# Optimization experiments

Hardware: AMD Instinct MI355X
Metric: run time of the kernel (lower is better)

Reference implementation:

```python
import jax, jax.numpy as jnp
import numpy as np
import math

D_MODEL = 512
N_HEADS = 8
BMIN, BMAX = 0.3, 1.0
W_E, W_M, W_I = 0.4, 0.4, 0.2


def norm_minmax(t):
    t_min = t.min(axis=-1, keepdims=True)
    t_max = t.max(axis=-1, keepdims=True)
    return (t - t_min) / jnp.maximum(t_max - t_min, 1e-8)


def setup_inputs() -> dict:
    key = jax.random.key(0)
    ks = jax.random.split(key, 12)
    B, S, D, C = 2, 2048, D_MODEL, 1000
    x = jax.random.normal(ks[0], (B, S, D), dtype=jnp.float32)
    out_probs = jax.nn.softmax(jax.random.normal(ks[1], (B, C), dtype=jnp.float32), axis=-1)
    idf_seq = jax.random.uniform(ks[2], (B, S), dtype=jnp.float32)
    def lin(kw, kb):
        W = jax.random.normal(kw, (D, D), dtype=jnp.float32) * 0.02
        b = jax.random.normal(kb, (D,), dtype=jnp.float32) * 0.02
        return W, b
    Wq, bq = lin(ks[3], ks[4])
    Wk, bk = lin(ks[5], ks[6])
    Wv, bv = lin(ks[7], ks[8])
    Wo, bo = lin(ks[9], ks[10])
    return dict(x=x, out_probs=out_probs, idf_seq=idf_seq,
                Wq=Wq, bq=bq, Wk=Wk, bk=bk, Wv=Wv, bv=bv, Wo=Wo, bo=bo)


def reference(x, out_probs, idf_seq, Wq, bq, Wk, bk, Wv, bv, Wo, bo):
    B, S, D = x.shape
    H = N_HEADS
    dk = D // H

    def heads(W, b):
        # (B,S,D) -> (B,H,S,dk)
        return (x @ W.T + b).reshape(B, S, H, dk).swapaxes(1, 2)

    q = heads(Wq, bq)
    k = heads(Wk, bk)
    v = heads(Wv, bv)

    logits = jnp.einsum('bhqd,bhkd->bhqk', q, k) / math.sqrt(dk)
    attn_probs = jax.nn.softmax(logits, axis=-1)  # (B,H,S,S)

    # --- compute_load ---
    p = jnp.maximum(attn_probs, 1e-12)
    H_i = (-(p * jnp.log(p)).sum(axis=-1)).mean(axis=1)  # (B,S)
    H_i = norm_minmax(H_i)

    top2 = jax.lax.top_k(out_probs, 2)[0]  # (B,2)
    margin = jnp.maximum(top2[:, 0] - top2[:, 1], 0.0)[:, None]  # (B,1)
    margin = jnp.broadcast_to(margin, (B, S))
    margin = norm_minmax(margin)
    load_from_margin = 1.0 - margin

    L = W_E * H_i + W_M * load_from_margin + W_I * idf_seq
    L = norm_minmax(L)

    # --- map load to budget and cap ---
    Bgt = BMIN + (BMAX - BMIN) * L  # (B,S)
    row_sum = jnp.maximum(attn_probs.sum(axis=-1, keepdims=True), 1e-12)  # (B,H,S,1)
    scale = jnp.minimum(Bgt[:, None, :, None] / row_sum, 1.0)
    attn_probs = attn_probs * scale

    y = jnp.einsum('bhqk,bhkd->bhqd', attn_probs, v)  # (B,H,S,dk)
    y = y.swapaxes(1, 2).reshape(B, S, D)
    y = y @ Wo.T + bo
    return y, attn_probs
```

## Files before the change

### kernel.cpp

```cpp
#include <hip/hip_runtime.h>
#include <hip/hip_bf16.h>


typedef __attribute__((ext_vector_type(8))) short bf16x8;
typedef __attribute__((ext_vector_type(4))) float f32x4;

static __device__ __forceinline__ unsigned short f2b(float f) {
  union { float f; unsigned int u; } v; v.f = f;
  unsigned int u = v.u;
  u += 0x7FFF + ((u >> 16) & 1);
  return (unsigned short)(u >> 16);
}

__global__ __launch_bounds__(256) void cvt_all(
    const float* __restrict__ x,
    const float* __restrict__ Wq, const float* __restrict__ Wk,
    const float* __restrict__ Wv, const float* __restrict__ Wo,
    unsigned short* __restrict__ xb, unsigned short* __restrict__ wqkv,
    unsigned short* __restrict__ wob)
{
  int i = blockIdx.x * 256 + threadIdx.x;
  const float* s; unsigned short* d; int off;
  if (i < 524288) { s = x; d = xb; off = i; }
  else {
    int j = i - 524288; int w = j >> 16; off = j & 65535;
    switch (w) {
      case 0: s = Wq; d = wqkv; break;
      case 1: s = Wk; d = wqkv + 262144; break;
      case 2: s = Wv; d = wqkv + 524288; break;
      default: s = Wo; d = wob; break;
    }
  }
  float4 v = reinterpret_cast<const float4*>(s)[off];
  ushort4 o;
  o.x = f2b(v.x); o.y = f2b(v.y); o.z = f2b(v.z); o.w = f2b(v.w);
  reinterpret_cast<ushort4*>(d)[off] = o;
}

__global__ __launch_bounds__(256) void qkv_gemm(
    const unsigned short* __restrict__ xb, const unsigned short* __restrict__ w,
    const float* __restrict__ bq, const float* __restrict__ bk, const float* __restrict__ bv,
    unsigned short* __restrict__ Qb, unsigned short* __restrict__ Kb,
    unsigned short* __restrict__ Vtb)
{
  __shared__ unsigned short smem[5120];
  unsigned short* shA = smem;
  unsigned short* shB = smem + 2560;
  const int tid = threadIdx.x;
  const int bm = blockIdx.x, bn = blockIdx.y;
  const int lane = tid & 63, wid = tid >> 6;
  const int wr = wid >> 1, wc = wid & 1;
  const int lg = lane >> 4, lc = lane & 15;

  f32x4 acc[2][2];
#pragma unroll
  for (int i = 0; i < 2; ++i)
#pragma unroll
    for (int j = 0; j < 2; ++j) acc[i][j] = f32x4{0.f, 0.f, 0.f, 0.f};

  const int row_st = tid >> 2;
  const int k8 = (tid & 3) * 8;
  for (int kt = 0; kt < 16; ++kt) {
    *reinterpret_cast<uint4*>(&shA[row_st * 40 + k8]) =
        *reinterpret_cast<const uint4*>(&xb[(size_t)(bm * 64 + row_st) * 512 + kt * 32 + k8]);
    *reinterpret_cast<uint4*>(&shB[row_st * 40 + k8]) =
        *reinterpret_cast<const uint4*>(&w[(size_t)(bn * 64 + row_st) * 512 + kt * 32 + k8]);
    __syncthreads();
    bf16x8 af[2], bfr[2];
#pragma unroll
    for (int f = 0; f < 2; ++f) {
      af[f]  = *reinterpret_cast<const bf16x8*>(&shA[(wr * 32 + f * 16 + lc) * 40 + lg * 8]);
      bfr[f] = *reinterpret_cast<const bf16x8*>(&shB[(wc * 32 + f * 16 + lc) * 40 + lg * 8]);
    }
#pragma unroll
    for (int fm = 0; fm < 2; ++fm)
#pragma unroll
      for (int fn = 0; fn < 2; ++fn)
        acc[fm][fn] = __builtin_amdgcn_mfma_f32_16x16x32_bf16(af[fm], bfr[fn], acc[fm][fn], 0, 0, 0);
    __syncthreads();
  }

  if (bn < 16) {
#pragma unroll
    for (int fm = 0; fm < 2; ++fm)
#pragma unroll
      for (int fn = 0; fn < 2; ++fn)
#pragma unroll
        for (int r = 0; r < 4; ++r) {
          int mi = bm * 64 + wr * 32 + fm * 16 + lg * 4 + r;
          int ni = bn * 64 + wc * 32 + fn * 16 + lc;
          int bb = mi >> 11, s = mi & 2047;
          float v = acc[fm][fn][r];
          if (ni < 512) {
            int h = ni >> 6, d = ni & 63;
            v = (v + bq[ni]) * 0.125f;
            Qb[(((size_t)bb * 8 + h) * 2048 + s) * 64 + d] = f2b(v);
          } else {
            int i2 = ni - 512; int h = i2 >> 6, d = i2 & 63;
            v += bk[i2];
            Kb[(((size_t)bb * 8 + h) * 2048 + s) * 64 + d] = f2b(v);
          }
        }
  } else {
    unsigned short (*T)[80] = reinterpret_cast<unsigned short(*)[80]>(smem);
    __syncthreads();
#pragma unroll
    for (int fm = 0; fm < 2; ++fm)
#pragma unroll
      for (int fn = 0; fn < 2; ++fn)
#pragma unroll
        for (int r = 0; r < 4; ++r) {
          int nl = wc * 32 + fn * 16 + lc;
          int ml = wr * 32 + fm * 16 + lg * 4 + r;
          int i2 = (bn - 16) * 64 + nl;
          T[nl][ml] = f2b(acc[fm][fn][r] + bv[i2]);
        }
    __syncthreads();
    const int row = tid >> 3;
    const int seg = tid & 7;
    const int h = bn - 16;
    int mi = bm * 64 + seg * 8;
    int bb = mi >> 11, s = mi & 2047;
#pragma unroll
    for (int rr = 0; rr < 2; ++rr) {
      int d = row + rr * 32;
      *reinterpret_cast<uint4*>(&Vtb[(((size_t)bb * 8 + h) * 64 + d) * 2048 + s]) =
          *reinterpret_cast<const uint4*>(&T[d][seg * 8]);
    }
  }
}

__global__ __launch_bounds__(256) void attn_pass1(
    const unsigned short* __restrict__ Qb, const unsigned short* __restrict__ Kb,
    float* __restrict__ zA, float* __restrict__ tA)
{
  __shared__ unsigned short Kbuf[2][4096];
  const int l = blockIdx.x;
  const int l2 = (l & 7) * 64 + (l >> 3);
  const int bh = l2 >> 5;
  const int qt = l2 & 31;
  const int tid = threadIdx.x;
  const int lane = tid & 63, wid = tid >> 6;
  const int lg = lane >> 4, lc = lane & 15;
  const int q0 = qt * 64 + wid * 16;
  const unsigned short* Qp = Qb + (size_t)bh * 2048 * 64;
  const unsigned short* Kp = Kb + (size_t)bh * 2048 * 64;
  bf16x8 aq0 = *reinterpret_cast<const bf16x8*>(&Qp[(q0 + lc) * 64 + lg * 8]);
  bf16x8 aq1 = *reinterpret_cast<const bf16x8*>(&Qp[(q0 + lc) * 64 + lg * 8 + 32]);

  const int srow = tid >> 3;
  const int sseg = tid & 7;
  const int wIdx0 = (srow * 64 + sseg * 8) ^ ((srow & 7) << 3);
  const int wIdx1 = wIdx0 + 2048;
  const int rswz = (lc & 7) << 3;

  float Z_[4], T_[4];
#pragma unroll
  for (int r = 0; r < 4; ++r) { Z_[r] = 0.f; T_[r] = 0.f; }

  {
    uint4 g0 = *reinterpret_cast<const uint4*>(&Kp[(size_t)srow * 64 + sseg * 8]);
    uint4 g1 = *reinterpret_cast<const uint4*>(&Kp[(size_t)(srow + 32) * 64 + sseg * 8]);
    *reinterpret_cast<uint4*>(&Kbuf[0][wIdx0]) = g0;
    *reinterpret_cast<uint4*>(&Kbuf[0][wIdx1]) = g1;
    __syncthreads();
  }

  for (int t = 0; t < 32; ++t) {
    uint4 g0, g1;
    if (t < 31) {
      g0 = *reinterpret_cast<const uint4*>(&Kp[(size_t)((t + 1) * 64 + srow) * 64 + sseg * 8]);
      g1 = *reinterpret_cast<const uint4*>(&Kp[(size_t)((t + 1) * 64 + srow + 32) * 64 + sseg * 8]);
    }
    const unsigned short* kb = Kbuf[t & 1];
    f32x4 acc[4];
#pragma unroll
    for (int c = 0; c < 4; ++c) {
      int rI = (c * 16 + lc) * 64;
      bf16x8 b0 = *reinterpret_cast<const bf16x8*>(&kb[(rI + lg * 8) ^ rswz]);
      bf16x8 b1 = *reinterpret_cast<const bf16x8*>(&kb[(rI + 32 + lg * 8) ^ rswz]);
      f32x4 z = {0.f, 0.f, 0.f, 0.f};
      z = __builtin_amdgcn_mfma_f32_16x16x32_bf16(aq0, b0, z, 0, 0, 0);
      acc[c] = __builtin_amdgcn_mfma_f32_16x16x32_bf16(aq1, b1, z, 0, 0, 0);
    }
#pragma unroll
    for (int r = 0; r < 4; ++r) {
#pragma unroll
      for (int c = 0; c < 4; ++c) {
        float lv = acc[c][r];
        float e = __expf(lv);
        Z_[r] += e;
        T_[r] = fmaf(lv, e, T_[r]);
      }
    }
    if (t < 31) {
      *reinterpret_cast<uint4*>(&Kbuf[(t + 1) & 1][wIdx0]) = g0;
      *reinterpret_cast<uint4*>(&Kbuf[(t + 1) & 1][wIdx1]) = g1;
    }
    __syncthreads();
  }
#pragma unroll
  for (int r = 0; r < 4; ++r) {
#pragma unroll
    for (int msk = 1; msk < 16; msk <<= 1) {
      Z_[r] += __shfl_xor(Z_[r], msk);
      T_[r] += __shfl_xor(T_[r], msk);
    }
  }
  if (lc == 0) {
#pragma unroll
    for (int r = 0; r < 4; ++r) {
      int idx = bh * 2048 + q0 + lg * 4 + r;
      zA[idx] = Z_[r]; tA[idx] = T_[r];
    }
  }
}

__global__ __launch_bounds__(256) void load_kernel(
    const float* __restrict__ zA, const float* __restrict__ tA,
    const float* __restrict__ idf, float* __restrict__ scaleArr)
{
  const int b = blockIdx.x, t = threadIdx.x;
  __shared__ float sh[2048];
  __shared__ float rmin[256], rmax[256];
  for (int s = t; s < 2048; s += 256) {
    float acc = 0.f;
    for (int h = 0; h < 8; ++h) {
      int idx = (b * 8 + h) * 2048 + s;
      float Z = zA[idx];
      acc += logf(Z) - tA[idx] / Z;
    }
    sh[s] = acc * 0.125f;
  }
  __syncthreads();
  float mn = 3e38f, mx = -3e38f;
  for (int s = t; s < 2048; s += 256) { float v = sh[s]; mn = fminf(mn, v); mx = fmaxf(mx, v); }
  rmin[t] = mn; rmax[t] = mx; __syncthreads();
  for (int o = 128; o > 0; o >>= 1) {
    if (t < o) { rmin[t] = fminf(rmin[t], rmin[t + o]); rmax[t] = fmaxf(rmax[t], rmax[t + o]); }
    __syncthreads();
  }
  float Hmin = rmin[0], Hmax = rmax[0];
  __syncthreads();
  for (int s = t; s < 2048; s += 256) {
    float Hn = (sh[s] - Hmin) / fmaxf(Hmax - Hmin, 1e-8f);
    sh[s] = 0.4f * Hn + 0.4f + 0.2f * idf[b * 2048 + s];
  }
  __syncthreads();
  mn = 3e38f; mx = -3e38f;
  for (int s = t; s < 2048; s += 256) { float v = sh[s]; mn = fminf(mn, v); mx = fmaxf(mx, v); }
  rmin[t] = mn; rmax[t] = mx; __syncthreads();
  for (int o = 128; o > 0; o >>= 1) {
    if (t < o) { rmin[t] = fminf(rmin[t], rmin[t + o]); rmax[t] = fmaxf(rmax[t], rmax[t + o]); }
    __syncthreads();
  }
  float Lmin = rmin[0], Lmax = rmax[0];
  for (int s = t; s < 2048; s += 256) {
    float Ln = (sh[s] - Lmin) / fmaxf(Lmax - Lmin, 1e-8f);
    scaleArr[b * 2048 + s] = fminf(0.3f + 0.7f * Ln, 1.0f);
  }
}

__global__ __launch_bounds__(256) void attn_pass2(
    const unsigned short* __restrict__ Qb, const unsigned short* __restrict__ Kb,
    const unsigned short* __restrict__ Vtb,
    const float* __restrict__ zA, const float* __restrict__ scaleArr,
    float* __restrict__ attnOut, unsigned short* __restrict__ yh)
{
  __shared__ unsigned short Kbuf[2][4096];
  __shared__ unsigned short Vbuf[2][4096];
  __shared__ unsigned short Pb[4][16 * 72];
  const int l = blockIdx.x;
  const int l2 = (l & 7) * 64 + (l >> 3);
  const int bh = l2 >> 5;
  const int qt = l2 & 31;
  const int b = bh >> 3; const int h = bh & 7;
  const int tid = threadIdx.x;
  const int lane = tid & 63, wid = tid >> 6;
  const int lg = lane >> 4, lc = lane & 15;
  const int q0 = qt * 64 + wid * 16;
  const unsigned short* Qp = Qb + (size_t)bh * 2048 * 64;
  const unsigned short* Kp = Kb + (size_t)bh * 2048 * 64;
  const unsigned short* Vp = Vtb + (size_t)bh * 64 * 2048;
  bf16x8 aq0 = *reinterpret_cast<const bf16x8*>(&Qp[(q0 + lc) * 64 + lg * 8]);
  bf16x8 aq1 = *reinterpret_cast<const bf16x8*>(&Qp[(q0 + lc) * 64 + lg * 8 + 32]);
  float coef[4];
#pragma unroll
  for (int r = 0; r < 4; ++r) {
    int q = q0 + lg * 4 + r;
    coef[r] = scaleArr[b * 2048 + q] / zA[bh * 2048 + q];
  }
  f32x4 accY[4];
#pragma unroll
  for (int i = 0; i < 4; ++i) accY[i] = f32x4{0.f, 0.f, 0.f, 0.f};
  unsigned short* myP = Pb[wid];
  float* aBase = attnOut + (size_t)bh * 2048 * 2048;

  const int srow = tid >> 3, sseg = tid & 7;
  const int wIdx0 = (srow * 64 + sseg * 8) ^ ((srow & 7) << 3);
  const int wIdx1 = wIdx0 + 2048;
  const int rswz = (lc & 7) << 3;

  {
    uint4 k0_ = *reinterpret_cast<const uint4*>(&Kp[(size_t)srow * 64 + sseg * 8]);
    uint4 k1_ = *reinterpret_cast<const uint4*>(&Kp[(size_t)(srow + 32) * 64 + sseg * 8]);
    uint4 v0_ = *reinterpret_cast<const uint4*>(&Vp[(size_t)srow * 2048 + sseg * 8]);
    uint4 v1_ = *reinterpret_cast<const uint4*>(&Vp[(size_t)(srow + 32) * 2048 + sseg * 8]);
    *reinterpret_cast<uint4*>(&Kbuf[0][wIdx0]) = k0_;
    *reinterpret_cast<uint4*>(&Kbuf[0][wIdx1]) = k1_;
    *reinterpret_cast<uint4*>(&Vbuf[0][wIdx0]) = v0_;
    *reinterpret_cast<uint4*>(&Vbuf[0][wIdx1]) = v1_;
    __syncthreads();
  }

  for (int t = 0; t < 32; ++t) {
    uint4 gk0, gk1, gv0, gv1;
    if (t < 31) {
      int kn = (t + 1) * 64;
      gk0 = *reinterpret_cast<const uint4*>(&Kp[(size_t)(kn + srow) * 64 + sseg * 8]);
      gk1 = *reinterpret_cast<const uint4*>(&Kp[(size_t)(kn + srow + 32) * 64 + sseg * 8]);
      gv0 = *reinterpret_cast<const uint4*>(&Vp[(size_t)srow * 2048 + kn + sseg * 8]);
      gv1 = *reinterpret_cast<const uint4*>(&Vp[(size_t)(srow + 32) * 2048 + kn + sseg * 8]);
    }
    const unsigned short* kb = Kbuf[t & 1];
    const unsigned short* vb = Vbuf[t & 1];
    f32x4 acc[4];
#pragma unroll
    for (int c = 0; c < 4; ++c) {
      int rI = (c * 16 + lc) * 64;
      bf16x8 b0 = *reinterpret_cast<const bf16x8*>(&kb[(rI + lg * 8) ^ rswz]);
      bf16x8 b1 = *reinterpret_cast<const bf16x8*>(&kb[(rI + 32 + lg * 8) ^ rswz]);
      f32x4 z = {0.f, 0.f, 0.f, 0.f};
      z = __builtin_amdgcn_mfma_f32_16x16x32_bf16(aq0, b0, z, 0, 0, 0);
      acc[c] = __builtin_amdgcn_mfma_f32_16x16x32_bf16(aq1, b1, z, 0, 0, 0);
    }
    const int k0g = t * 64;
#pragma unroll
    for (int c = 0; c < 4; ++c)
#pragma unroll
      for (int r = 0; r < 4; ++r) {
        float pv = __expf(acc[c][r]) * coef[r];
        int qrow = q0 + lg * 4 + r;
        aBase[(size_t)qrow * 2048 + k0g + c * 16 + lc] = pv;
        myP[(lg * 4 + r) * 72 + c * 16 + lc] = f2b(pv);
      }
#pragma unroll
    for (int kk = 0; kk < 2; ++kk) {
      bf16x8 ap = *reinterpret_cast<const bf16x8*>(&myP[lc * 72 + kk * 32 + lg * 8]);
#pragma unroll
      for (int cf = 0; cf < 4; ++cf) {
        int rI = (cf * 16 + lc) * 64;
        bf16x8 bv_ = *reinterpret_cast<const bf16x8*>(&vb[(rI + kk * 32 + lg * 8) ^ rswz]);
        accY[cf] = __builtin_amdgcn_mfma_f32_16x16x32_bf16(ap, bv_, accY[cf], 0, 0, 0);
      }
    }
    if (t < 31) {
      *reinterpret_cast<uint4*>(&Kbuf[(t + 1) & 1][wIdx0]) = gk0;
      *reinterpret_cast<uint4*>(&Kbuf[(t + 1) & 1][wIdx1]) = gk1;
      *reinterpret_cast<uint4*>(&Vbuf[(t + 1) & 1][wIdx0]) = gv0;
      *reinterpret_cast<uint4*>(&Vbuf[(t + 1) & 1][wIdx1]) = gv1;
    }
    __syncthreads();
  }
#pragma unroll
  for (int cf = 0; cf < 4; ++cf)
#pragma unroll
    for (int r = 0; r < 4; ++r) {
      int qrow = q0 + lg * 4 + r;
      yh[((size_t)b * 2048 + qrow) * 512 + h * 64 + cf * 16 + lc] = f2b(accY[cf][r]);
    }
}

__global__ __launch_bounds__(256) void out_gemm(
    const unsigned short* __restrict__ yhb, const unsigned short* __restrict__ wo,
    const float* __restrict__ bo, float* __restrict__ yOut)
{
  __shared__ unsigned short shA[64 * 40];
  __shared__ unsigned short shB[64 * 40];
  const int tid = threadIdx.x;
  const int bm = blockIdx.x, bn = blockIdx.y;
  const int lane = tid & 63, wid = tid >> 6;
  const int wr = wid >> 1, wc = wid & 1;
  const int lg = lane >> 4, lc = lane & 15;

  f32x4 acc[2][2];
#pragma unroll
  for (int i = 0; i < 2; ++i)
#pragma unroll
    for (int j = 0; j < 2; ++j) acc[i][j] = f32x4{0.f, 0.f, 0.f, 0.f};

  const int row_st = tid >> 2;
  const int k8 = (tid & 3) * 8;
  for (int kt = 0; kt < 16; ++kt) {
    *reinterpret_cast<uint4*>(&shA[row_st * 40 + k8]) =
        *reinterpret_cast<const uint4*>(&yhb[(size_t)(bm * 64 + row_st) * 512 + kt * 32 + k8]);
    *reinterpret_cast<uint4*>(&shB[row_st * 40 + k8]) =
        *reinterpret_cast<const uint4*>(&wo[(size_t)(bn * 64 + row_st) * 512 + kt * 32 + k8]);
    __syncthreads();
    bf16x8 af[2], bfr[2];
#pragma unroll
    for (int f = 0; f < 2; ++f) {
      af[f]  = *reinterpret_cast<const bf16x8*>(&shA[(wr * 32 + f * 16 + lc) * 40 + lg * 8]);
      bfr[f] = *reinterpret_cast<const bf16x8*>(&shB[(wc * 32 + f * 16 + lc) * 40 + lg * 8]);
    }
#pragma unroll
    for (int fm = 0; fm < 2; ++fm)
#pragma unroll
      for (int fn = 0; fn < 2; ++fn)
        acc[fm][fn] = __builtin_amdgcn_mfma_f32_16x16x32_bf16(af[fm], bfr[fn], acc[fm][fn], 0, 0, 0);
    __syncthreads();
  }
#pragma unroll
  for (int fm = 0; fm < 2; ++fm)
#pragma unroll
    for (int fn = 0; fn < 2; ++fn)
#pragma unroll
      for (int r = 0; r < 4; ++r) {
        int mi = bm * 64 + wr * 32 + fm * 16 + lg * 4 + r;
        int ni = bn * 64 + wc * 32 + fn * 16 + lc;
        yOut[(size_t)mi * 512 + ni] = acc[fm][fn][r] + bo[ni];
      }
}

extern "C" void kernel_launch(void* const* d_in, const int* in_sizes, int n_in,
                              void* d_out, int out_size, void* d_ws, size_t ws_size,
                              hipStream_t stream) {
  const float* x   = (const float*)d_in[0];
  const float* idf = (const float*)d_in[2];
  const float* Wq = (const float*)d_in[3];
  const float* bq = (const float*)d_in[4];
  const float* Wk = (const float*)d_in[5];
  const float* bk = (const float*)d_in[6];
  const float* Wv = (const float*)d_in[7];
  const float* bv = (const float*)d_in[8];
  const float* Wo = (const float*)d_in[9];
  const float* bo = (const float*)d_in[10];

  float* yOut = (float*)d_out;
  float* attnOut = yOut + (size_t)2 * 2048 * 512;

  char* p = (char*)d_ws;
  auto alloc = [&](size_t bytes) { char* r = p; p += (bytes + 255) & ~(size_t)255; return r; };
  unsigned short* xb   = (unsigned short*)alloc((size_t)2097152 * 2);
  unsigned short* wqkv = (unsigned short*)alloc((size_t)786432 * 2);
  unsigned short* wob  = (unsigned short*)alloc((size_t)262144 * 2);
  unsigned short* Qb   = (unsigned short*)alloc((size_t)2097152 * 2);
  unsigned short* Kb   = (unsigned short*)alloc((size_t)2097152 * 2);
  unsigned short* Vtb  = (unsigned short*)alloc((size_t)2097152 * 2);
  unsigned short* yh   = (unsigned short*)alloc((size_t)2097152 * 2);
  float* zA = (float*)alloc((size_t)32768 * 4);
  float* tA = (float*)alloc((size_t)32768 * 4);
  float* scaleArr = (float*)alloc((size_t)4096 * 4);

  cvt_all<<<3072, 256, 0, stream>>>(x, Wq, Wk, Wv, Wo, xb, wqkv, wob);
  qkv_gemm<<<dim3(64, 24), 256, 0, stream>>>(xb, wqkv, bq, bk, bv, Qb, Kb, Vtb);
  attn_pass1<<<512, 256, 0, stream>>>(Qb, Kb, zA, tA);
  load_kernel<<<2, 256, 0, stream>>>(zA, tA, idf, scaleArr);
  attn_pass2<<<512, 256, 0, stream>>>(Qb, Kb, Vtb, zA, scaleArr, attnOut, yh);
  out_gemm<<<dim3(64, 8), 256, 0, stream>>>(yh, wob, bo, yOut);
}
```

Measured before the change: 132.4 us.

## Move PV product into first attention pass and defer per-row scaling to output GEMM

The first pass now computes the unnormalized exp(logits)·V product along with the entropy sums, and stores it as fp32. The per-row coefficient scale/Z is applied while out_gemm loads that data. The second pass now only recomputes QK^T to write the scaled attention probabilities, and it stages them through LDS so the global stores are vectorized float4. This removes the V loads and PV MFMAs from the store-bound pass. The cost is an fp32 intermediate that doubles traffic for y, plus reusing the xb buffer as yacc, which relies on xb being dead after qkv_gemm. It also takes bf16 rounding of unnormalized exponentials, which could lose precision if the logits grow large.

Result: slower. 152.3 us (+15.0%).

```diff
diff --git a/kernel.cpp b/kernel.cpp
--- a/kernel.cpp
+++ b/kernel.cpp
@@ -132,140 +132,8 @@
 
 __global__ __launch_bounds__(256) void attn_pass1(
     const unsigned short* __restrict__ Qb, const unsigned short* __restrict__ Kb,
-    float* __restrict__ zA, float* __restrict__ tA)
-{
-  __shared__ unsigned short Kbuf[2][4096];
-  const int l = blockIdx.x;
-  const int l2 = (l & 7) * 64 + (l >> 3);
-  const int bh = l2 >> 5;
-  const int qt = l2 & 31;
-  const int tid = threadIdx.x;
-  const int lane = tid & 63, wid = tid >> 6;
-  const int lg = lane >> 4, lc = lane & 15;
-  const int q0 = qt * 64 + wid * 16;
-  const unsigned short* Qp = Qb + (size_t)bh * 2048 * 64;
-  const unsigned short* Kp = Kb + (size_t)bh * 2048 * 64;
-  bf16x8 aq0 = *reinterpret_cast<const bf16x8*>(&Qp[(q0 + lc) * 64 + lg * 8]);
-  bf16x8 aq1 = *reinterpret_cast<const bf16x8*>(&Qp[(q0 + lc) * 64 + lg * 8 + 32]);
-
-  const int srow = tid >> 3;
-  const int sseg = tid & 7;
-  const int wIdx0 = (srow * 64 + sseg * 8) ^ ((srow & 7) << 3);
-  const int wIdx1 = wIdx0 + 2048;
-  const int rswz = (lc & 7) << 3;
-
-  float Z_[4], T_[4];
-#pragma unroll
-  for (int r = 0; r < 4; ++r) { Z_[r] = 0.f; T_[r] = 0.f; }
-
-  {
-    uint4 g0 = *reinterpret_cast<const uint4*>(&Kp[(size_t)srow * 64 + sseg * 8]);
-    uint4 g1 = *reinterpret_cast<const uint4*>(&Kp[(size_t)(srow + 32) * 64 + sseg * 8]);
-    *reinterpret_cast<uint4*>(&Kbuf[0][wIdx0]) = g0;
-    *reinterpret_cast<uint4*>(&Kbuf[0][wIdx1]) = g1;
-    __syncthreads();
-  }
-
-  for (int t = 0; t < 32; ++t) {
-    uint4 g0, g1;
-    if (t < 31) {
-      g0 = *reinterpret_cast<const uint4*>(&Kp[(size_t)((t + 1) * 64 + srow) * 64 + sseg * 8]);
-      g1 = *reinterpret_cast<const uint4*>(&Kp[(size_t)((t + 1) * 64 + srow + 32) * 64 + sseg * 8]);
-    }
-    const unsigned short* kb = Kbuf[t & 1];
-    f32x4 acc[4];
-#pragma unroll
-    for (int c = 0; c < 4; ++c) {
-      int rI = (c * 16 + lc) * 64;
-      bf16x8 b0 = *reinterpret_cast<const bf16x8*>(&kb[(rI + lg * 8) ^ rswz]);
-      bf16x8 b1 = *reinterpret_cast<const bf16x8*>(&kb[(rI + 32 + lg * 8) ^ rswz]);
-      f32x4 z = {0.f, 0.f, 0.f, 0.f};
-      z = __builtin_amdgcn_mfma_f32_16x16x32_bf16(aq0, b0, z, 0, 0, 0);
-      acc[c] = __builtin_amdgcn_mfma_f32_16x16x32_bf16(aq1, b1, z, 0, 0, 0);
-    }
-#pragma unroll
-    for (int r = 0; r < 4; ++r) {
-#pragma unroll
-      for (int c = 0; c < 4; ++c) {
-        float lv = acc[c][r];
-        float e = __expf(lv);
-        Z_[r] += e;
-        T_[r] = fmaf(lv, e, T_[r]);
-      }
-    }
-    if (t < 31) {
-      *reinterpret_cast<uint4*>(&Kbuf[(t + 1) & 1][wIdx0]) = g0;
-      *reinterpret_cast<uint4*>(&Kbuf[(t + 1) & 1][wIdx1]) = g1;
-    }
-    __syncthreads();
-  }
-#pragma unroll
-  for (int r = 0; r < 4; ++r) {
-#pragma unroll
-    for (int msk = 1; msk < 16; msk <<= 1) {
-      Z_[r] += __shfl_xor(Z_[r], msk);
-      T_[r] += __shfl_xor(T_[r], msk);
-    }
-  }
-  if (lc == 0) {
-#pragma unroll
-    for (int r = 0; r < 4; ++r) {
-      int idx = bh * 2048 + q0 + lg * 4 + r;
-      zA[idx] = Z_[r]; tA[idx] = T_[r];
-    }
-  }
-}
-
-__global__ __launch_bounds__(256) void load_kernel(
-    const float* __restrict__ zA, const float* __restrict__ tA,
-    const float* __restrict__ idf, float* __restrict__ scaleArr)
-{
-  const int b = blockIdx.x, t = threadIdx.x;
-  __shared__ float sh[2048];
-  __shared__ float rmin[256], rmax[256];
-  for (int s = t; s < 2048; s += 256) {
-    float acc = 0.f;
-    for (int h = 0; h < 8; ++h) {
-      int idx = (b * 8 + h) * 2048 + s;
-      float Z = zA[idx];
-      acc += logf(Z) - tA[idx] / Z;
-    }
-    sh[s] = acc * 0.125f;
-  }
-  __syncthreads();
-  float mn = 3e38f, mx = -3e38f;
-  for (int s = t; s < 2048; s += 256) { float v = sh[s]; mn = fminf(mn, v); mx = fmaxf(mx, v); }
-  rmin[t] = mn; rmax[t] = mx; __syncthreads();
-  for (int o = 128; o > 0; o >>= 1) {
-    if (t < o) { rmin[t] = fminf(rmin[t], rmin[t + o]); rmax[t] = fmaxf(rmax[t], rmax[t + o]); }
-    __syncthreads();
-  }
-  float Hmin = rmin[0], Hmax = rmax[0];
-  __syncthreads();
-  for (int s = t; s < 2048; s += 256) {
-    float Hn = (sh[s] - Hmin) / fmaxf(Hmax - Hmin, 1e-8f);
-    sh[s] = 0.4f * Hn + 0.4f + 0.2f * idf[b * 2048 + s];
-  }
-  __syncthreads();
-  mn = 3e38f; mx = -3e38f;
-  for (int s = t; s < 2048; s += 256) { float v = sh[s]; mn = fminf(mn, v); mx = fmaxf(mx, v); }
-  rmin[t] = mn; rmax[t] = mx; __syncthreads();
-  for (int o = 128; o > 0; o >>= 1) {
-    if (t < o) { rmin[t] = fminf(rmin[t], rmin[t + o]); rmax[t] = fmaxf(rmax[t], rmax[t + o]); }
-    __syncthreads();
-  }
-  float Lmin = rmin[0], Lmax = rmax[0];
-  for (int s = t; s < 2048; s += 256) {
-    float Ln = (sh[s] - Lmin) / fmaxf(Lmax - Lmin, 1e-8f);
-    scaleArr[b * 2048 + s] = fminf(0.3f + 0.7f * Ln, 1.0f);
-  }
-}
-
-__global__ __launch_bounds__(256) void attn_pass2(
-    const unsigned short* __restrict__ Qb, const unsigned short* __restrict__ Kb,
     const unsigned short* __restrict__ Vtb,
-    const float* __restrict__ zA, const float* __restrict__ scaleArr,
-    float* __restrict__ attnOut, unsigned short* __restrict__ yh)
+    float* __restrict__ zA, float* __restrict__ tA, float* __restrict__ yacc)
 {
   __shared__ unsigned short Kbuf[2][4096];
   __shared__ unsigned short Vbuf[2][4096];
@@ -284,22 +152,19 @@
   const unsigned short* Vp = Vtb + (size_t)bh * 64 * 2048;
   bf16x8 aq0 = *reinterpret_cast<const bf16x8*>(&Qp[(q0 + lc) * 64 + lg * 8]);
   bf16x8 aq1 = *reinterpret_cast<const bf16x8*>(&Qp[(q0 + lc) * 64 + lg * 8 + 32]);
-  float coef[4];
-#pragma unroll
-  for (int r = 0; r < 4; ++r) {
-    int q = q0 + lg * 4 + r;
-    coef[r] = scaleArr[b * 2048 + q] / zA[bh * 2048 + q];
-  }
-  f32x4 accY[4];
-#pragma unroll
-  for (int i = 0; i < 4; ++i) accY[i] = f32x4{0.f, 0.f, 0.f, 0.f};
-  unsigned short* myP = Pb[wid];
-  float* aBase = attnOut + (size_t)bh * 2048 * 2048;
 
   const int srow = tid >> 3, sseg = tid & 7;
   const int wIdx0 = (srow * 64 + sseg * 8) ^ ((srow & 7) << 3);
   const int wIdx1 = wIdx0 + 2048;
   const int rswz = (lc & 7) << 3;
+
+  float Z_[4], T_[4];
+#pragma unroll
+  for (int r = 0; r < 4; ++r) { Z_[r] = 0.f; T_[r] = 0.f; }
+  f32x4 accY[4];
+#pragma unroll
+  for (int i = 0; i < 4; ++i) accY[i] = f32x4{0.f, 0.f, 0.f, 0.f};
+  unsigned short* myP = Pb[wid];
 
   {
     uint4 k0_ = *reinterpret_cast<const uint4*>(&Kp[(size_t)srow * 64 + sseg * 8]);
@@ -334,15 +199,15 @@
       z = __builtin_amdgcn_mfma_f32_16x16x32_bf16(aq0, b0, z, 0, 0, 0);
       acc[c] = __builtin_amdgcn_mfma_f32_16x16x32_bf16(aq1, b1, z, 0, 0, 0);
     }
-    const int k0g = t * 64;
 #pragma unroll
     for (int c = 0; c < 4; ++c)
 #pragma unroll
       for (int r = 0; r < 4; ++r) {
-        float pv = __expf(acc[c][r]) * coef[r];
-        int qrow = q0 + lg * 4 + r;
-        aBase[(size_t)qrow * 2048 + k0g + c * 16 + lc] = pv;
-        myP[(lg * 4 + r) * 72 + c * 16 + lc] = f2b(pv);
+        float lv = acc[c][r];
+        float e = __expf(lv);
+        Z_[r] += e;
+        T_[r] = fmaf(lv, e, T_[r]);
+        myP[(lg * 4 + r) * 72 + c * 16 + lc] = f2b(e);
       }
 #pragma unroll
     for (int kk = 0; kk < 2; ++kk) {
@@ -363,17 +228,157 @@
     __syncthreads();
   }
 #pragma unroll
+  for (int r = 0; r < 4; ++r) {
+#pragma unroll
+    for (int msk = 1; msk < 16; msk <<= 1) {
+      Z_[r] += __shfl_xor(Z_[r], msk);
+      T_[r] += __shfl_xor(T_[r], msk);
+    }
+  }
+  if (lc == 0) {
+#pragma unroll
+    for (int r = 0; r < 4; ++r) {
+      int idx = bh * 2048 + q0 + lg * 4 + r;
+      zA[idx] = Z_[r]; tA[idx] = T_[r];
+    }
+  }
+#pragma unroll
   for (int cf = 0; cf < 4; ++cf)
 #pragma unroll
     for (int r = 0; r < 4; ++r) {
       int qrow = q0 + lg * 4 + r;
-      yh[((size_t)b * 2048 + qrow) * 512 + h * 64 + cf * 16 + lc] = f2b(accY[cf][r]);
-    }
+      yacc[((size_t)b * 2048 + qrow) * 512 + h * 64 + cf * 16 + lc] = accY[cf][r];
+    }
+}
+
+__global__ __launch_bounds__(256) void load_kernel(
+    const float* __restrict__ zA, const float* __restrict__ tA,
+    const float* __restrict__ idf, float* __restrict__ scaleArr)
+{
+  const int b = blockIdx.x, t = threadIdx.x;
+  __shared__ float sh[2048];
+  __shared__ float rmin[256], rmax[256];
+  for (int s = t; s < 2048; s += 256) {
+    float acc = 0.f;
+    for (int h = 0; h < 8; ++h) {
+      int idx = (b * 8 + h) * 2048 + s;
+      float Z = zA[idx];
+      acc += logf(Z) - tA[idx] / Z;
+    }
+    sh[s] = acc * 0.125f;
+  }
+  __syncthreads();
+  float mn = 3e38f, mx = -3e38f;
+  for (int s = t; s < 2048; s += 256) { float v = sh[s]; mn = fminf(mn, v); mx = fmaxf(mx, v); }
+  rmin[t] = mn; rmax[t] = mx; __syncthreads();
+  for (int o = 128; o > 0; o >>= 1) {
+    if (t < o) { rmin[t] = fminf(rmin[t], rmin[t + o]); rmax[t] = fmaxf(rmax[t], rmax[t + o]); }
+    __syncthreads();
+  }
+  float Hmin = rmin[0], Hmax = rmax[0];
+  __syncthreads();
+  for (int s = t; s < 2048; s += 256) {
+    float Hn = (sh[s] - Hmin) / fmaxf(Hmax - Hmin, 1e-8f);
+    sh[s] = 0.4f * Hn + 0.4f + 0.2f * idf[b * 2048 + s];
+  }
+  __syncthreads();
+  mn = 3e38f; mx = -3e38f;
+  for (int s = t; s < 2048; s += 256) { float v = sh[s]; mn = fminf(mn, v); mx = fmaxf(mx, v); }
+  rmin[t] = mn; rmax[t] = mx; __syncthreads();
+  for (int o = 128; o > 0; o >>= 1) {
+    if (t < o) { rmin[t] = fminf(rmin[t], rmin[t + o]); rmax[t] = fmaxf(rmax[t], rmax[t + o]); }
+    __syncthreads();
+  }
+  float Lmin = rmin[0], Lmax = rmax[0];
+  for (int s = t; s < 2048; s += 256) {
+    float Ln = (sh[s] - Lmin) / fmaxf(Lmax - Lmin, 1e-8f);
+    scaleArr[b * 2048 + s] = fminf(0.3f + 0.7f * Ln, 1.0f);
+  }
+}
+
+__global__ __launch_bounds__(256) void attn_pass2(
+    const unsigned short* __restrict__ Qb, const unsigned short* __restrict__ Kb,
+    const float* __restrict__ zA, const float* __restrict__ scaleArr,
+    float* __restrict__ attnOut)
+{
+  __shared__ unsigned short Kbuf[2][4096];
+  __shared__ float Pf[4][16 * 68];
+  const int l = blockIdx.x;
+  const int l2 = (l & 7) * 64 + (l >> 3);
+  const int bh = l2 >> 5;
+  const int qt = l2 & 31;
+  const int b = bh >> 3;
+  const int tid = threadIdx.x;
+  const int lane = tid & 63, wid = tid >> 6;
+  const int lg = lane >> 4, lc = lane & 15;
+  const int q0 = qt * 64 + wid * 16;
+  const unsigned short* Qp = Qb + (size_t)bh * 2048 * 64;
+  const unsigned short* Kp = Kb + (size_t)bh * 2048 * 64;
+  bf16x8 aq0 = *reinterpret_cast<const bf16x8*>(&Qp[(q0 + lc) * 64 + lg * 8]);
+  bf16x8 aq1 = *reinterpret_cast<const bf16x8*>(&Qp[(q0 + lc) * 64 + lg * 8 + 32]);
+  float coef[4];
+#pragma unroll
+  for (int r = 0; r < 4; ++r) {
+    int q = q0 + lg * 4 + r;
+    coef[r] = scaleArr[b * 2048 + q] / zA[bh * 2048 + q];
+  }
+  float* myP = Pf[wid];
+  float* aBase = attnOut + (size_t)bh * 2048 * 2048;
+
+  const int srow = tid >> 3, sseg = tid & 7;
+  const int wIdx0 = (srow * 64 + sseg * 8) ^ ((srow & 7) << 3);
+  const int wIdx1 = wIdx0 + 2048;
+  const int rswz = (lc & 7) << 3;
+
+  {
+    uint4 k0_ = *reinterpret_cast<const uint4*>(&Kp[(size_t)srow * 64 + sseg * 8]);
+    uint4 k1_ = *reinterpret_cast<const uint4*>(&Kp[(size_t)(srow + 32) * 64 + sseg * 8]);
+    *reinterpret_cast<uint4*>(&Kbuf[0][wIdx0]) = k0_;
+    *reinterpret_cast<uint4*>(&Kbuf[0][wIdx1]) = k1_;
+    __syncthreads();
+  }
+
+  for (int t = 0; t < 32; ++t) {
+    uint4 gk0, gk1;
+    if (t < 31) {
+      int kn = (t + 1) * 64;
+      gk0 = *reinterpret_cast<const uint4*>(&Kp[(size_t)(kn + srow) * 64 + sseg * 8]);
+      gk1 = *reinterpret_cast<const uint4*>(&Kp[(size_t)(kn + srow + 32) * 64 + sseg * 8]);
+    }
+    const unsigned short* kb = Kbuf[t & 1];
+    f32x4 acc[4];
+#pragma unroll
+    for (int c = 0; c < 4; ++c) {
+      int rI = (c * 16 + lc) * 64;
+      bf16x8 b0 = *reinterpret_cast<const bf16x8*>(&kb[(rI + lg * 8) ^ rswz]);
+      bf16x8 b1 = *reinterpret_cast<const bf16x8*>(&kb[(rI + 32 + lg * 8) ^ rswz]);
+      f32x4 z = {0.f, 0.f, 0.f, 0.f};
+      z = __builtin_amdgcn_mfma_f32_16x16x32_bf16(aq0, b0, z, 0, 0, 0);
+      acc[c] = __builtin_amdgcn_mfma_f32_16x16x32_bf16(aq1, b1, z, 0, 0, 0);
+    }
+#pragma unroll
+    for (int c = 0; c < 4; ++c)
+#pragma unroll
+      for (int r = 0; r < 4; ++r)
+        myP[(lg * 4 + r) * 68 + c * 16 + lc] = __expf(acc[c][r]) * coef[r];
+    const int k0g = t * 64;
+#pragma unroll
+    for (int j = 0; j < 4; ++j) {
+      f32x4 v = *reinterpret_cast<const f32x4*>(&myP[(j * 4 + lg) * 68 + lc * 4]);
+      *reinterpret_cast<f32x4*>(&aBase[(size_t)(q0 + j * 4 + lg) * 2048 + k0g + lc * 4]) = v;
+    }
+    if (t < 31) {
+      *reinterpret_cast<uint4*>(&Kbuf[(t + 1) & 1][wIdx0]) = gk0;
+      *reinterpret_cast<uint4*>(&Kbuf[(t + 1) & 1][wIdx1]) = gk1;
+    }
+    __syncthreads();
+  }
 }
 
 __global__ __launch_bounds__(256) void out_gemm(
-    const unsigned short* __restrict__ yhb, const unsigned short* __restrict__ wo,
-    const float* __restrict__ bo, float* __restrict__ yOut)
+    const float* __restrict__ yacc, const unsigned short* __restrict__ wo,
+    const float* __restrict__ bo, const float* __restrict__ zA,
+    const float* __restrict__ scaleArr, float* __restrict__ yOut)
 {
   __shared__ unsigned short shA[64 * 40];
   __shared__ unsigned short shB[64 * 40];
@@ -391,9 +396,20 @@
 
   const int row_st = tid >> 2;
   const int k8 = (tid & 3) * 8;
+  const int m = bm * 64 + row_st;
+  const int bb = m >> 11, s = m & 2047;
+  const float scl = scaleArr[bb * 2048 + s];
   for (int kt = 0; kt < 16; ++kt) {
-    *reinterpret_cast<uint4*>(&shA[row_st * 40 + k8]) =
-        *reinterpret_cast<const uint4*>(&yhb[(size_t)(bm * 64 + row_st) * 512 + kt * 32 + k8]);
+    const int h = kt >> 1;
+    float coefA = scl / zA[((size_t)bb * 8 + h) * 2048 + s];
+    float4 v0 = *reinterpret_cast<const float4*>(&yacc[(size_t)m * 512 + kt * 32 + k8]);
+    float4 v1 = *reinterpret_cast<const float4*>(&yacc[(size_t)m * 512 + kt * 32 + k8 + 4]);
+    uint4 pk;
+    pk.x = (unsigned)f2b(v0.x * coefA) | ((unsigned)f2b(v0.y * coefA) << 16);
+    pk.y = (unsigned)f2b(v0.z * coefA) | ((unsigned)f2b(v0.w * coefA) << 16);
+    pk.z = (unsigned)f2b(v1.x * coefA) | ((unsigned)f2b(v1.y * coefA) << 16);
+    pk.w = (unsigned)f2b(v1.z * coefA) | ((unsigned)f2b(v1.w * coefA) << 16);
+    *reinterpret_cast<uint4*>(&shA[row_st * 40 + k8]) = pk;
     *reinterpret_cast<uint4*>(&shB[row_st * 40 + k8]) =
         *reinterpret_cast<const uint4*>(&wo[(size_t)(bn * 64 + row_st) * 512 + kt * 32 + k8]);
     __syncthreads();
@@ -441,21 +457,22 @@
 
   char* p = (char*)d_ws;
   auto alloc = [&](size_t bytes) { char* r = p; p += (bytes + 255) & ~(size_t)255; return r; };
-  unsigned short* xb   = (unsigned short*)alloc((size_t)2097152 * 2);
   unsigned short* wqkv = (unsigned short*)alloc((size_t)786432 * 2);
   unsigned short* wob  = (unsigned short*)alloc((size_t)262144 * 2);
   unsigned short* Qb   = (unsigned short*)alloc((size_t)2097152 * 2);
   unsigned short* Kb   = (unsigned short*)alloc((size_t)2097152 * 2);
   unsigned short* Vtb  = (unsigned short*)alloc((size_t)2097152 * 2);
-  unsigned short* yh   = (unsigned short*)alloc((size_t)2097152 * 2);
   float* zA = (float*)alloc((size_t)32768 * 4);
   float* tA = (float*)alloc((size_t)32768 * 4);
   float* scaleArr = (float*)alloc((size_t)4096 * 4);
+  char* tail = alloc((size_t)2097152 * 4);
+  unsigned short* xb = (unsigned short*)tail;
+  float* yacc = (float*)tail;
 
   cvt_all<<<3072, 256, 0, stream>>>(x, Wq, Wk, Wv, Wo, xb, wqkv, wob);
   qkv_gemm<<<dim3(64, 24), 256, 0, stream>>>(xb, wqkv, bq, bk, bv, Qb, Kb, Vtb);
-  attn_pass1<<<512, 256, 0, stream>>>(Qb, Kb, zA, tA);
+  attn_pass1<<<512, 256, 0, stream>>>(Qb, Kb, Vtb, zA, tA, yacc);
   load_kernel<<<2, 256, 0, stream>>>(zA, tA, idf, scaleArr);
-  attn_pass2<<<512, 256, 0, stream>>>(Qb, Kb, Vtb, zA, scaleArr, attnOut, yh);
-  out_gemm<<<dim3(64, 8), 256, 0, stream>>>(yh, wob, bo, yOut);
-}
+  out_gemm<<<dim3(64, 8), 256, 0, stream>>>(yacc, wob, bo, zA, scaleArr, yOut);
+  attn_pass2<<<512, 256, 0, stream>>>(Qb, Kb, zA, scaleArr, attnOut);
+}
```
